# Kernel optimization log

Hardware: AMD Instinct MI355X
Metric: run time of the kernel (lower is better)

The kernel has to match this reference:

```python
import jax, jax.numpy as jnp
import numpy as np

N = 50000   # nodes
E = 600000  # edges
D = 128     # in_feats = n_hidden
B = 16384   # pair batch
L = 2       # n_layers
C = 2       # n_classes
EPS = 1e-5


def setup_inputs() -> dict:
    key = jax.random.key(0)
    ks = jax.random.split(key, 16)
    s = 0.05
    return {
        "h": jax.random.normal(ks[0], (N, D), jnp.float32),
        "edge_src": jax.random.randint(ks[1], (E,), 0, N),
        "edge_dst": jax.random.randint(ks[2], (E,), 0, N),
        "x1": jax.random.randint(ks[3], (B,), 0, N),
        "x2": jax.random.randint(ks[4], (B,), 0, N),
        "x1_tar": jax.random.randint(ks[5], (B,), 0, N),
        "x2_tar": jax.random.randint(ks[6], (B,), 0, N),
        # SAGEConv params (mean aggregator): rst = h@W_self + mean_neigh@W_neigh + b
        "W_self": jax.random.normal(ks[7], (L, D, D), jnp.float32) * s,
        "W_neigh": jax.random.normal(ks[8], (L, D, D), jnp.float32) * s,
        "b_conv": jnp.zeros((L, D), jnp.float32),
        # head: linear1(3D->D) -> BN -> relu -> linear2(D->C)
        "W1": jax.random.normal(ks[9], (3 * D, D), jnp.float32) * s,
        "b1": jnp.zeros((D,), jnp.float32),
        "gamma": jnp.ones((D,), jnp.float32),
        "beta": jnp.zeros((D,), jnp.float32),
        "W2": jax.random.normal(ks[10], (D, C), jnp.float32) * s,
        "b2": jnp.zeros((C,), jnp.float32),
    }


def _sage_layers(h, edge_src, edge_dst, W_self, W_neigh, b_conv):
    # in-degree for mean aggregation (clamped to 1 to avoid div by 0)
    deg = jax.ops.segment_sum(jnp.ones((E,), h.dtype), edge_dst, num_segments=N)
    deg = jnp.maximum(deg, 1.0)[:, None]
    for l in range(L):
        msg = h[edge_src]                                        # [E, D] gather
        agg = jax.ops.segment_sum(msg, edge_dst, num_segments=N) / deg  # [N, D]
        h = jax.nn.relu(h @ W_self[l] + agg @ W_neigh[l] + b_conv[l])
    return h


def _pair_feat(h, a, b):
    ha, hb = h[a], h[b]
    return jnp.concatenate([ha, hb, jnp.abs(ha - hb)], axis=1)  # [B, 3D]


def _batchnorm(x, gamma, beta):
    m = x.mean(axis=0)
    v = x.var(axis=0)  # biased variance, as torch BN in training mode normalization
    return (x - m) * jax.lax.rsqrt(v + EPS) * gamma + beta


def reference(h, edge_src, edge_dst, x1, x2, x1_tar, x2_tar,
              W_self, W_neigh, b_conv, W1, b1, gamma, beta, W2, b2):
    h = _sage_layers(h, edge_src, edge_dst, W_self, W_neigh, b_conv)
    h_src = _pair_feat(h, x1, x2) @ W1 + b1
    h_tar = _pair_feat(h, x1_tar, x2_tar) @ W1 + b1
    h_src = _batchnorm(h_src, gamma, beta)
    h_tar = _batchnorm(h_tar, gamma, beta)
    h_src_mmd = jax.nn.relu(h_src)
    h_tar_mmd = jax.nn.relu(h_tar)
    h_p = h_src_mmd @ W2 + b2
    return (h_p, h_src_mmd, h_tar_mmd)
```

## Files before the change

kernel.cpp:

```cpp
#include <hip/hip_runtime.h>

#define NN 50000
#define NE 600000
#define DF 128
#define NB 16384

typedef short bf16x8 __attribute__((ext_vector_type(8)));
typedef float f32x4 __attribute__((ext_vector_type(4)));

__device__ __forceinline__ float bf2f(unsigned short u){
  return __uint_as_float(((unsigned int)u) << 16);
}
__device__ __forceinline__ unsigned short f2bf(float x){
  unsigned int b = __float_as_uint(x);
  return (unsigned short)((b + 0x7FFFu + ((b >> 16) & 1u)) >> 16);
}

__global__ void GraphSAGE_8504035246140_kernel(){ }

__global__ __launch_bounds__(256) void k_prelude(
    const float* h_in, unsigned short* h_c,
    const float* Ws, const float* Wn, const float* W1,
    unsigned short* WsB, unsigned short* WnB, unsigned short* W1B,
    int* cnt, float* stats){
  int b = blockIdx.x, t = threadIdx.x;
  if (b < 3125){
    int i = b * 256 + t;
    const float4* s = (const float4*)h_in;
    float4 v0 = s[i * 2], v1 = s[i * 2 + 1];
    unsigned short d[8] = {f2bf(v0.x), f2bf(v0.y), f2bf(v0.z), f2bf(v0.w),
                           f2bf(v1.x), f2bf(v1.y), f2bf(v1.z), f2bf(v1.w)};
    *(bf16x8*)(h_c + i * 8) = *(bf16x8*)d;
  } else if (b < 3516){
    int i = (b - 3125) * 256 + t;
    if (i < 2 * NN) cnt[i] = 0;
  } else if (b < 3518){
    int i = (b - 3516) * 256 + t;
    if (i < 512) stats[i] = 0.f;
  } else {
    int idx = (b - 3518) * 256 + t;
    if (idx < 2 * DF * DF){
      int layer = idx >> 14;
      int e = idx & (DF * DF - 1);
      int k = e >> 7, n = e & 127;
      int dst = layer * DF * DF + (((k >> 3) * 128 + n) << 3) + (k & 7);
      WsB[dst] = f2bf(Ws[idx]);
      WnB[dst] = f2bf(Wn[idx]);
    }
    if (idx < 3 * DF * DF){
      int k = idx >> 7, n = idx & 127;
      W1B[(((k >> 3) * 128 + n) << 3) + (k & 7)] = f2bf(W1[idx]);
    }
  }
}

__global__ void k_hist(const int* dst, int* cnt){
  int e = blockIdx.x * 256 + threadIdx.x;
  if (e < NE) atomicAdd(&cnt[dst[e]], 1);
}
__global__ void k_scan1(const int* cnt, int* bsum){
  __shared__ int l[256];
  int t = threadIdx.x, i = blockIdx.x * 256 + t;
  l[t] = (i < NN) ? cnt[i] : 0;
  __syncthreads();
  for (int o = 128; o > 0; o >>= 1){
    if (t < o) l[t] += l[t + o];
    __syncthreads();
  }
  if (t == 0) bsum[blockIdx.x] = l[0];
}
__global__ void k_scan3(const int* cnt, const int* bsum, int* rp, float* dinv){
  __shared__ int bs[256];
  __shared__ int l[256];
  int t = threadIdx.x, i = blockIdx.x * 256 + t;
  bs[t] = (t < 196) ? bsum[t] : 0;
  int v = (i < NN) ? cnt[i] : 0;
  l[t] = v;
  __syncthreads();
  for (int o = 1; o < 256; o <<= 1){
    int xb = (t >= o) ? bs[t - o] : 0;
    int xl = (t >= o) ? l[t - o] : 0;
    __syncthreads();
    bs[t] += xb; l[t] += xl;
    __syncthreads();
  }
  int base = (blockIdx.x == 0) ? 0 : bs[blockIdx.x - 1];
  if (i < NN){
    rp[i] = base + l[t] - v;
    dinv[i] = 1.0f / fmaxf((float)v, 1.0f);
    if (i == NN - 1) rp[NN] = base + l[t];
  }
}
__global__ void k_scatter(const int* src, const int* dst,
                          const int* rp, int* fill, int* perm){
  int e = blockIdx.x * 256 + threadIdx.x;
  if (e < NE){
    int d = dst[e];
    int pos = atomicAdd(&fill[d], 1);
    perm[rp[d] + pos] = src[e];
  }
}

__global__ __launch_bounds__(256) void k_agg(
    const unsigned int* hb32, const int* rp, const int* perm,
    const float* dinv, unsigned int* agg32){
  int n = blockIdx.x * 4 + (threadIdx.x >> 6);
  if (n >= NN) return;
  int l = threadIdx.x & 63;
  int half = l >> 5, lh = l & 31;
  int s = rp[n], e = rp[n + 1];
  float a0 = 0.f, a1 = 0.f, a2 = 0.f, a3 = 0.f;
  int i = s;
  for (; i + 8 <= e; i += 8){
    int p0 = perm[i + 0 + half];
    int p1 = perm[i + 2 + half];
    int p2 = perm[i + 4 + half];
    int p3 = perm[i + 6 + half];
    uint2 x0 = *(const uint2*)(hb32 + (size_t)p0 * 64 + lh * 2);
    uint2 x1 = *(const uint2*)(hb32 + (size_t)p1 * 64 + lh * 2);
    uint2 x2 = *(const uint2*)(hb32 + (size_t)p2 * 64 + lh * 2);
    uint2 x3 = *(const uint2*)(hb32 + (size_t)p3 * 64 + lh * 2);
    a0 += __uint_as_float(x0.x << 16); a1 += __uint_as_float(x0.x & 0xffff0000u);
    a2 += __uint_as_float(x0.y << 16); a3 += __uint_as_float(x0.y & 0xffff0000u);
    a0 += __uint_as_float(x1.x << 16); a1 += __uint_as_float(x1.x & 0xffff0000u);
    a2 += __uint_as_float(x1.y << 16); a3 += __uint_as_float(x1.y & 0xffff0000u);
    a0 += __uint_as_float(x2.x << 16); a1 += __uint_as_float(x2.x & 0xffff0000u);
    a2 += __uint_as_float(x2.y << 16); a3 += __uint_as_float(x2.y & 0xffff0000u);
    a0 += __uint_as_float(x3.x << 16); a1 += __uint_as_float(x3.x & 0xffff0000u);
    a2 += __uint_as_float(x3.y << 16); a3 += __uint_as_float(x3.y & 0xffff0000u);
  }
  for (; i < e; i += 2){
    if (i + half < e){
      int p = perm[i + half];
      uint2 x = *(const uint2*)(hb32 + (size_t)p * 64 + lh * 2);
      a0 += __uint_as_float(x.x << 16); a1 += __uint_as_float(x.x & 0xffff0000u);
      a2 += __uint_as_float(x.y << 16); a3 += __uint_as_float(x.y & 0xffff0000u);
    }
  }
  a0 += __shfl_xor(a0, 32);
  a1 += __shfl_xor(a1, 32);
  a2 += __shfl_xor(a2, 32);
  a3 += __shfl_xor(a3, 32);
  if (half == 0){
    float di = dinv[n];
    uint2 r;
    r.x = (unsigned int)f2bf(a0 * di) | ((unsigned int)f2bf(a1 * di) << 16);
    r.y = (unsigned int)f2bf(a2 * di) | ((unsigned int)f2bf(a3 * di) << 16);
    *(uint2*)(agg32 + (size_t)n * 64 + lh * 2) = r;
  }
}

__global__ __launch_bounds__(256) void k_layer_mfma(
    const unsigned short* hb, const unsigned short* aggb,
    const unsigned short* WsB, const unsigned short* WnB,
    const float* bias, unsigned short* hout){
  int t = threadIdx.x;
  int w = t >> 6, l = t & 63;
  int m = l & 15, q = l >> 4;
  int r0 = blockIdx.x * 64 + w * 16;
  int arow = r0 + m; if (arow > NN - 1) arow = NN - 1;
  const unsigned short* hp = hb   + (size_t)arow * DF + q * 8;
  const unsigned short* ap = aggb + (size_t)arow * DF + q * 8;
  f32x4 acc[8];
  for (int ct = 0; ct < 8; ++ct){
    float bbc = bias[ct * 16 + m];
    acc[ct] = (f32x4){bbc, bbc, bbc, bbc};
  }
  for (int kt = 0; kt < 4; ++kt){
    bf16x8 a_h = *(const bf16x8*)(hp + kt * 32);
    bf16x8 a_g = *(const bf16x8*)(ap + kt * 32);
    int kg = kt * 4 + q;
    for (int ct = 0; ct < 8; ++ct){
      bf16x8 b_s = *(const bf16x8*)(WsB + (((kg << 7) + ct * 16 + m) << 3));
      bf16x8 b_n = *(const bf16x8*)(WnB + (((kg << 7) + ct * 16 + m) << 3));
      acc[ct] = __builtin_amdgcn_mfma_f32_16x16x32_bf16(a_h, b_s, acc[ct], 0, 0, 0);
      acc[ct] = __builtin_amdgcn_mfma_f32_16x16x32_bf16(a_g, b_n, acc[ct], 0, 0, 0);
    }
  }
  for (int ct = 0; ct < 8; ++ct){
    int col = ct * 16 + m;
    for (int reg = 0; reg < 4; ++reg){
      int row = r0 + q * 4 + reg;
      if (row < NN) hout[(size_t)row * DF + col] = f2bf(fmaxf(acc[ct][reg], 0.f));
    }
  }
}

__global__ __launch_bounds__(256) void k_pair_mfma(
    const unsigned short* h2,
    const int* x1, const int* x2, const int* x1t, const int* x2t,
    const unsigned short* W1B, const float* b1, float* zbase, float* stats){
  __shared__ __align__(16) unsigned short F[64 * 392];
  __shared__ float csum[128], csq[128];
  int g = blockIdx.y;
  const int* ia = g ? x1t : x1;
  const int* ib = g ? x2t : x2;
  float* z = zbase + (size_t)g * NB * DF;
  int t = threadIdx.x;
  if (t < 128){ csum[t] = 0.f; csq[t] = 0.f; }
  int r0 = blockIdx.x * 64;
  int i = t >> 2, qq = t & 3;
  int r = r0 + i;
  int a = ia[r], b = ib[r];
  const unsigned short* pa = h2 + (size_t)a * DF + qq * 32;
  const unsigned short* pb = h2 + (size_t)b * DF + qq * 32;
  unsigned short* fr = F + i * 392;
  for (int jj = 0; jj < 4; ++jj){
    bf16x8 va = *(const bf16x8*)(pa + jj * 8);
    bf16x8 vb = *(const bf16x8*)(pb + jj * 8);
    *(bf16x8*)(fr + qq * 32 + jj * 8) = va;
    *(bf16x8*)(fr + 128 + qq * 32 + jj * 8) = vb;
    unsigned short d[8];
    for (int e = 0; e < 8; ++e){
      float fa = bf2f((unsigned short)va[e]);
      float fb = bf2f((unsigned short)vb[e]);
      d[e] = f2bf(fabsf(fa - fb));
    }
    *(bf16x8*)(fr + 256 + qq * 32 + jj * 8) = *(bf16x8*)d;
  }
  __syncthreads();
  int w = t >> 6, l = t & 63;
  int m = l & 15, q = l >> 4;
  int rl = w * 16 + m;
  f32x4 acc[8];
  for (int ct = 0; ct < 8; ++ct){
    float bbc = b1[ct * 16 + m];
    acc[ct] = (f32x4){bbc, bbc, bbc, bbc};
  }
  for (int kt = 0; kt < 12; ++kt){
    bf16x8 af = *(const bf16x8*)(F + rl * 392 + kt * 32 + q * 8);
    int kg = kt * 4 + q;
    for (int ct = 0; ct < 8; ++ct){
      bf16x8 bfr = *(const bf16x8*)(W1B + (((kg << 7) + ct * 16 + m) << 3));
      acc[ct] = __builtin_amdgcn_mfma_f32_16x16x32_bf16(af, bfr, acc[ct], 0, 0, 0);
    }
  }
  for (int ct = 0; ct < 8; ++ct){
    int col = ct * 16 + m;
    int row = r0 + w * 16 + q * 4;
    float s = 0.f, s2 = 0.f;
    for (int reg = 0; reg < 4; ++reg){
      float v = acc[ct][reg];
      z[(size_t)(row + reg) * DF + col] = v;
      s += v; s2 += v * v;
    }
    atomicAdd(&csum[col], s);
    atomicAdd(&csq[col], s2);
  }
  __syncthreads();
  if (t < 128){
    atomicAdd(&stats[g * 256 + t], csum[t]);
    atomicAdd(&stats[g * 256 + 128 + t], csq[t]);
  }
}

__global__ __launch_bounds__(256) void k_norm_hp(
    const float* zbase, const float* stats,
    const float* gamma, const float* beta,
    const float* W2, const float* b2, float* mmd_base, float* hp){
  __shared__ float s0[256], s1[256];
  int g = blockIdx.y;
  int t = threadIdx.x;
  int rl = t >> 7, c = t & 127;
  int row = blockIdx.x * 2 + rl;
  float m = stats[g * 256 + c] / (float)NB;
  float v = stats[g * 256 + 128 + c] / (float)NB - m * m;
  float istd = 1.0f / sqrtf(v + 1e-5f);
  size_t off = (size_t)g * NB * DF + (size_t)row * DF + c;
  float y = fmaxf((zbase[off] - m) * istd * gamma[c] + beta[c], 0.f);
  mmd_base[off] = y;
  if (g == 0){
    s0[t] = y * W2[c * 2];
    s1[t] = y * W2[c * 2 + 1];
    __syncthreads();
    int base = rl << 7;
    for (int o = 64; o > 0; o >>= 1){
      if (c < o){ s0[base + c] += s0[base + c + o]; s1[base + c] += s1[base + c + o]; }
      __syncthreads();
    }
    if (c == 0){
      hp[row * 2]     = s0[base] + b2[0];
      hp[row * 2 + 1] = s1[base] + b2[1];
    }
  }
}

extern "C" __attribute__((used, visibility("default")))
void kernel_launch(void* const* d_in, const int* in_sizes, int n_in,
                   void* d_out, int out_size, void* d_ws, size_t ws_size,
                   hipStream_t stream){
  const float* h_in  = (const float*)d_in[0];
  const int* esrc = (const int*)d_in[1];
  const int* edst = (const int*)d_in[2];
  const int* x1   = (const int*)d_in[3];
  const int* x2   = (const int*)d_in[4];
  const int* x1t  = (const int*)d_in[5];
  const int* x2t  = (const int*)d_in[6];
  const float* Wself = (const float*)d_in[7];
  const float* Wneigh= (const float*)d_in[8];
  const float* bconv = (const float*)d_in[9];
  const float* W1    = (const float*)d_in[10];
  const float* b1    = (const float*)d_in[11];
  const float* gamma = (const float*)d_in[12];
  const float* beta  = (const float*)d_in[13];
  const float* W2    = (const float*)d_in[14];
  const float* b2    = (const float*)d_in[15];
  float* out = (float*)d_out;
  float* hp_out   = out;
  float* mmd_base = out + 2 * NB;

  float* zreg  = (float*)d_ws;
  unsigned short* aggb = (unsigned short*)zreg;
  float* stats = zreg + (size_t)2 * NB * DF;
  float* mstd  = stats + 512;
  float* dinv  = mstd + 512;
  int* cnt  = (int*)(dinv + 50048);
  int* fill = cnt + NN;
  int* rp   = fill + NN;
  int* perm = rp + 50016;
  int* bsum = perm + 600000;
  unsigned short* h_c = (unsigned short*)(bsum + 256);
  unsigned short* h1b = h_c + (size_t)NN * DF;
  unsigned short* h2b = h_c;
  unsigned short* WsB = h1b + (size_t)NN * DF;
  unsigned short* WnB = WsB + 2 * DF * DF;
  unsigned short* W1B = WnB + 2 * DF * DF;

  k_prelude<<<3710, 256, 0, stream>>>(h_in, h_c, Wself, Wneigh, W1,
                                      WsB, WnB, W1B, cnt, stats);

  k_hist<<<(NE + 255) / 256, 256, 0, stream>>>(edst, cnt);
  k_scan1<<<196, 256, 0, stream>>>(cnt, bsum);
  k_scan3<<<196, 256, 0, stream>>>(cnt, bsum, rp, dinv);
  k_scatter<<<(NE + 255) / 256, 256, 0, stream>>>(esrc, edst, rp, fill, perm);

  k_agg<<<(NN + 3) / 4, 256, 0, stream>>>((const unsigned int*)h_c, rp, perm,
                                          dinv, (unsigned int*)aggb);
  k_layer_mfma<<<(NN + 63) / 64, 256, 0, stream>>>(h_c, aggb, WsB, WnB, bconv, h1b);
  k_agg<<<(NN + 3) / 4, 256, 0, stream>>>((const unsigned int*)h1b, rp, perm,
                                          dinv, (unsigned int*)aggb);
  k_layer_mfma<<<(NN + 63) / 64, 256, 0, stream>>>(h1b, aggb, WsB + DF * DF,
                                                   WnB + DF * DF, bconv + DF, h2b);

  k_pair_mfma<<<dim3(NB / 64, 2), 256, 0, stream>>>(h2b, x1, x2, x1t, x2t,
                                                    W1B, b1, zreg, stats);
  k_norm_hp<<<dim3(NB / 2, 2), 256, 0, stream>>>(zreg, stats, gamma, beta,
                                                 W2, b2, mmd_base, hp_out);
}
```

Before: 302.2 us.

## Fuse pair GEMM with batchnorm and head via cooperative grid sync

Merges the pair-feature GEMM and the batchnorm/relu/linear2 kernel into one cooperative kernel. A grid-wide sync waits for the global column statistics, then each block normalizes its accumulator registers directly, so the fp32 z intermediate is never written to or read back from global memory. The h_p reduction now uses wavefront shuffles instead of shared-memory tree reductions. It also rewrites the aggregation tail loop to issue four predicated gathers at once. The cooperative launch needs all 512 blocks resident at the same time, and the grid sync adds a barrier cost.

```diff
diff --git a/kernel.cpp b/kernel.cpp
--- a/kernel.cpp
+++ b/kernel.cpp
@@ -1,4 +1,5 @@
 #include <hip/hip_runtime.h>
+#include <hip/hip_cooperative_groups.h>
 
 #define NN 50000
 #define NE 600000
@@ -129,12 +130,31 @@
     a0 += __uint_as_float(x3.x << 16); a1 += __uint_as_float(x3.x & 0xffff0000u);
     a2 += __uint_as_float(x3.y << 16); a3 += __uint_as_float(x3.y & 0xffff0000u);
   }
-  for (; i < e; i += 2){
-    if (i + half < e){
-      int p = perm[i + half];
-      uint2 x = *(const uint2*)(hb32 + (size_t)p * 64 + lh * 2);
-      a0 += __uint_as_float(x.x << 16); a1 += __uint_as_float(x.x & 0xffff0000u);
-      a2 += __uint_as_float(x.y << 16); a3 += __uint_as_float(x.y & 0xffff0000u);
+  if (i < e){
+    int i0 = i + 0 + half, i1 = i + 2 + half, i2 = i + 4 + half, i3 = i + 6 + half;
+    int p0 = perm[i0 < e ? i0 : s];
+    int p1 = perm[i1 < e ? i1 : s];
+    int p2 = perm[i2 < e ? i2 : s];
+    int p3 = perm[i3 < e ? i3 : s];
+    uint2 x0 = *(const uint2*)(hb32 + (size_t)p0 * 64 + lh * 2);
+    uint2 x1 = *(const uint2*)(hb32 + (size_t)p1 * 64 + lh * 2);
+    uint2 x2 = *(const uint2*)(hb32 + (size_t)p2 * 64 + lh * 2);
+    uint2 x3 = *(const uint2*)(hb32 + (size_t)p3 * 64 + lh * 2);
+    if (i0 < e){
+      a0 += __uint_as_float(x0.x << 16); a1 += __uint_as_float(x0.x & 0xffff0000u);
+      a2 += __uint_as_float(x0.y << 16); a3 += __uint_as_float(x0.y & 0xffff0000u);
+    }
+    if (i1 < e){
+      a0 += __uint_as_float(x1.x << 16); a1 += __uint_as_float(x1.x & 0xffff0000u);
+      a2 += __uint_as_float(x1.y << 16); a3 += __uint_as_float(x1.y & 0xffff0000u);
+    }
+    if (i2 < e){
+      a0 += __uint_as_float(x2.x << 16); a1 += __uint_as_float(x2.x & 0xffff0000u);
+      a2 += __uint_as_float(x2.y << 16); a3 += __uint_as_float(x2.y & 0xffff0000u);
+    }
+    if (i3 < e){
+      a0 += __uint_as_float(x3.x << 16); a1 += __uint_as_float(x3.x & 0xffff0000u);
+      a2 += __uint_as_float(x3.y << 16); a3 += __uint_as_float(x3.y & 0xffff0000u);
     }
   }
   a0 += __shfl_xor(a0, 32);
@@ -186,16 +206,18 @@
   }
 }
 
-__global__ __launch_bounds__(256) void k_pair_mfma(
+__global__ __launch_bounds__(256) void k_pair_bn_hp(
     const unsigned short* h2,
     const int* x1, const int* x2, const int* x1t, const int* x2t,
-    const unsigned short* W1B, const float* b1, float* zbase, float* stats){
+    const unsigned short* W1B, const float* b1,
+    const float* gamma, const float* beta,
+    const float* W2, const float* b2,
+    float* stats, float* mmd_base, float* hp){
   __shared__ __align__(16) unsigned short F[64 * 392];
   __shared__ float csum[128], csq[128];
   int g = blockIdx.y;
   const int* ia = g ? x1t : x1;
   const int* ib = g ? x2t : x2;
-  float* z = zbase + (size_t)g * NB * DF;
   int t = threadIdx.x;
   if (t < 128){ csum[t] = 0.f; csq[t] = 0.f; }
   int r0 = blockIdx.x * 64;
@@ -237,11 +259,9 @@
   }
   for (int ct = 0; ct < 8; ++ct){
     int col = ct * 16 + m;
-    int row = r0 + w * 16 + q * 4;
     float s = 0.f, s2 = 0.f;
     for (int reg = 0; reg < 4; ++reg){
       float v = acc[ct][reg];
-      z[(size_t)(row + reg) * DF + col] = v;
       s += v; s2 += v * v;
     }
     atomicAdd(&csum[col], s);
@@ -252,35 +272,38 @@
     atomicAdd(&stats[g * 256 + t], csum[t]);
     atomicAdd(&stats[g * 256 + 128 + t], csq[t]);
   }
-}
-
-__global__ __launch_bounds__(256) void k_norm_hp(
-    const float* zbase, const float* stats,
-    const float* gamma, const float* beta,
-    const float* W2, const float* b2, float* mmd_base, float* hp){
-  __shared__ float s0[256], s1[256];
-  int g = blockIdx.y;
-  int t = threadIdx.x;
-  int rl = t >> 7, c = t & 127;
-  int row = blockIdx.x * 2 + rl;
-  float m = stats[g * 256 + c] / (float)NB;
-  float v = stats[g * 256 + 128 + c] / (float)NB - m * m;
-  float istd = 1.0f / sqrtf(v + 1e-5f);
-  size_t off = (size_t)g * NB * DF + (size_t)row * DF + c;
-  float y = fmaxf((zbase[off] - m) * istd * gamma[c] + beta[c], 0.f);
-  mmd_base[off] = y;
-  if (g == 0){
-    s0[t] = y * W2[c * 2];
-    s1[t] = y * W2[c * 2 + 1];
-    __syncthreads();
-    int base = rl << 7;
-    for (int o = 64; o > 0; o >>= 1){
-      if (c < o){ s0[base + c] += s0[base + c + o]; s1[base + c] += s1[base + c + o]; }
-      __syncthreads();
-    }
-    if (c == 0){
-      hp[row * 2]     = s0[base] + b2[0];
-      hp[row * 2 + 1] = s1[base] + b2[1];
+  cooperative_groups::this_grid().sync();
+  float sc[8], of[8], w20[8], w21[8];
+  for (int ct = 0; ct < 8; ++ct){
+    int col = ct * 16 + m;
+    float mm = stats[g * 256 + col] * (1.0f / NB);
+    float vv = stats[g * 256 + 128 + col] * (1.0f / NB) - mm * mm;
+    float istd = 1.0f / sqrtf(vv + 1e-5f);
+    sc[ct] = istd * gamma[col];
+    of[ct] = beta[col] - mm * sc[ct];
+    w20[ct] = W2[col * 2];
+    w21[ct] = W2[col * 2 + 1];
+  }
+  float* mmd = mmd_base + (size_t)g * NB * DF;
+  int rowbase = r0 + w * 16 + q * 4;
+  for (int reg = 0; reg < 4; ++reg){
+    int row = rowbase + reg;
+    float s0 = 0.f, s1 = 0.f;
+    for (int ct = 0; ct < 8; ++ct){
+      float y = fmaxf(acc[ct][reg] * sc[ct] + of[ct], 0.f);
+      mmd[(size_t)row * DF + ct * 16 + m] = y;
+      s0 += y * w20[ct];
+      s1 += y * w21[ct];
+    }
+    if (g == 0){
+      for (int o = 8; o > 0; o >>= 1){
+        s0 += __shfl_xor(s0, o);
+        s1 += __shfl_xor(s1, o);
+      }
+      if (m == 0){
+        hp[row * 2]     = s0 + b2[0];
+        hp[row * 2 + 1] = s1 + b2[1];
+      }
     }
   }
 }
@@ -342,8 +365,17 @@
   k_layer_mfma<<<(NN + 63) / 64, 256, 0, stream>>>(h1b, aggb, WsB + DF * DF,
                                                    WnB + DF * DF, bconv + DF, h2b);
 
-  k_pair_mfma<<<dim3(NB / 64, 2), 256, 0, stream>>>(h2b, x1, x2, x1t, x2t,
-                                                    W1B, b1, zreg, stats);
-  k_norm_hp<<<dim3(NB / 2, 2), 256, 0, stream>>>(zreg, stats, gamma, beta,
-                                                 W2, b2, mmd_base, hp_out);
-}
+  {
+    const unsigned short* h2b_ = h2b;
+    const int* x1_ = x1; const int* x2_ = x2;
+    const int* x1t_ = x1t; const int* x2t_ = x2t;
+    const unsigned short* W1B_ = W1B;
+    const float* b1_ = b1; const float* gamma_ = gamma; const float* beta_ = beta;
+    const float* W2_ = W2; const float* b2_ = b2;
+    float* stats_ = stats; float* mmd_ = mmd_base; float* hp_ = hp_out;
+    void* args[] = {&h2b_, &x1_, &x2_, &x1t_, &x2t_, &W1B_, &b1_,
+                    &gamma_, &beta_, &W2_, &b2_, &stats_, &mmd_, &hp_};
+    hipLaunchCooperativeKernel((void*)k_pair_bn_hp, dim3(NB / 64, 2), dim3(256),
+                               args, 0, stream);
+  }
+}
```

New measurement: 380.6 us. 1.26x slower.
